# Performance work log

Hardware: AMD Instinct MI355X
Metric: run time of the kernel (lower is better)

The kernel has to match this reference:

```python
import jax, jax.numpy as jnp
import numpy as np

COMMITMENT_COST = 0.25


def setup_inputs() -> dict:
    key = jax.random.key(0)
    k1, k2 = jax.random.split(key)
    B, D, H, W = 16, 256, 64, 64   # channel-first latents, D == embedding_dim
    K = 1024                        # num_embeddings
    z = jax.random.normal(k1, (B, D, H, W), dtype=jnp.float32)
    emb = jax.random.normal(k2, (K, D), dtype=jnp.float32)
    emb = emb / jnp.linalg.norm(emb, axis=1, keepdims=True)  # F.normalize(p=2, dim=1)
    return {"z": z, "embeddings": emb}


def reference(z, embeddings):
    D = embeddings.shape[1]
    input_shape = z.shape
    flat_z = z.reshape(-1, D)  # matches torch .view(-1, embedding_dim) on contiguous tensor
    dist = (jnp.sum(flat_z * flat_z, axis=1, keepdims=True)
            + jnp.sum(embeddings * embeddings, axis=1)
            - 2.0 * flat_z @ embeddings.T)
    encoding_indices = jnp.argmin(dist, axis=1)                       # [N]
    # one-hot @ embeddings == gather (same math, no [N,K] one-hot materialized)
    quantized = embeddings[encoding_indices].reshape(input_shape)
    e_latent_loss = jnp.mean((jax.lax.stop_gradient(quantized) - z) ** 2)
    q_latent_loss = jnp.mean((quantized - jax.lax.stop_gradient(z)) ** 2)
    vq_loss = q_latent_loss + COMMITMENT_COST * e_latent_loss
    quantized_st = z + jax.lax.stop_gradient(quantized - z)  # straight-through
    encoding_indices = encoding_indices.reshape((input_shape[0],) + input_shape[2:])
    return quantized_st, vq_loss, encoding_indices
```

## Files before the change

### kernel.cpp

```cpp
#include <hip/hip_runtime.h>
#include <stdint.h>


typedef __attribute__((ext_vector_type(8))) short short8;
typedef __attribute__((ext_vector_type(16))) float f32x16;

#define THR_S 1e-3f
#define WLCAP 16384

__device__ __forceinline__ unsigned short f2bf(float f) {
    const unsigned int x = __float_as_uint(f);
    return (unsigned short)((x + 0x7FFFu + ((x >> 16) & 1u)) >> 16);
}
__device__ __forceinline__ float bf2f(unsigned short h) {
    return __uint_as_float(((unsigned int)h) << 16);
}

#define MFMA32(A, B, C) __builtin_amdgcn_mfma_f32_32x32x16_bf16(A, B, C, 0, 0, 0)

__global__ __launch_bounds__(256)
void eprep_kernel(const float* __restrict__ emb, unsigned short* __restrict__ eh_t,
                  unsigned short* __restrict__ el_t, float* __restrict__ enorm,
                  int* __restrict__ wlcnt) {
    const int code = blockIdx.x;
    const int k = threadIdx.x;
    if (code == 0 && k == 0) wlcnt[0] = 0;
    const float v = emb[code * 256 + k];
    const unsigned short h = f2bf(v);
    const int idx = ((k >> 4) << 14) + (code << 4) + (((k >> 3) & 1) << 3) + (k & 7);
    eh_t[idx] = h;
    el_t[idx] = f2bf(v - bf2f(h));
    float s = v * v;
#pragma unroll
    for (int o = 32; o > 0; o >>= 1) s += __shfl_xor(s, o);
    __shared__ float red[4];
    if ((k & 63) == 0) red[k >> 6] = s;
    __syncthreads();
    if (k == 0) enorm[code] = (red[0] + red[1]) + (red[2] + red[3]);
}

#define UPD(S, C, B1, I1, B2) { \
    const bool lt_ = (S) < B1; \
    B2 = lt_ ? B1 : fminf(B2, (S)); \
    I1 = lt_ ? (C) : I1; \
    B1 = lt_ ? (S) : B1; }

#define MERGE32(B1, I1, B2) { \
    const float ob1_ = __shfl_xor(B1, 32); \
    const int   oi1_ = __shfl_xor(I1, 32); \
    const float ob2_ = __shfl_xor(B2, 32); \
    const float nb2_ = fminf(fminf(B2, ob2_), fmaxf(B1, ob1_)); \
    if (ob1_ < B1 || (ob1_ == B1 && oi1_ < I1)) { B1 = ob1_; I1 = oi1_; } \
    B2 = nb2_; }

#define PFLOAD(S, U) { \
    const int un_ = (U) & 63; \
    const int ofs_ = ((un_ & 15) << 15) + ((un_ >> 4) << 10); \
    pf##S##h = *reinterpret_cast<const short8*>(ehp + ofs_); \
    pf##S##l = *reinterpret_cast<const short8*>(elp + ofs_); }

#define UNIT(S, KS) { \
    const int ko_ = (((KS) << 5) + (hi << 4)) ^ rsw; \
    const short8 bh0 = *reinterpret_cast<const short8*>(zbuf + rb0 + ko_); \
    const short8 bl0 = *reinterpret_cast<const short8*>(zbuf + 32768 + rb0 + ko_); \
    const short8 bh1 = *reinterpret_cast<const short8*>(zbuf + rb1 + ko_); \
    const short8 bl1 = *reinterpret_cast<const short8*>(zbuf + 32768 + rb1 + ko_); \
    acc1a = MFMA32(pf##S##h, bh0, acc1a); \
    acc1b = MFMA32(pf##S##h, bh1, acc1b); \
    acc2a = MFMA32(pf##S##h, bl0, acc2a); \
    acc2b = MFMA32(pf##S##h, bl1, acc2b); \
    acc2a = MFMA32(pf##S##l, bh0, acc2a); \
    acc2b = MFMA32(pf##S##l, bh1, acc2b); }

__global__ __launch_bounds__(512, 4)
void argmin_kernel(const float* __restrict__ z, const unsigned short* __restrict__ eh_t,
                   float* __restrict__ idx_out, int* __restrict__ wl,
                   int* __restrict__ wlcnt, const float* __restrict__ emb,
                   float* __restrict__ q_out, float* __restrict__ partials) {
    __shared__ char zbuf[65536];
    __shared__ float m_b1[8][64];
    __shared__ int   m_i1[8][64];
    __shared__ float m_b2[8][64];
    __shared__ int   fidx_s[64];

    const int t = threadIdx.x;
    const int l = t & 63;
    const int w = t >> 6;
    const int cl = l & 31;
    const int hi = l >> 5;

    const float* zblk = z + (size_t)blockIdx.x * 16384;

#pragma unroll
    for (int i = 0; i < 8; ++i) {
        const int idx = i * 2048 + t * 4;
        const int row = idx >> 8, k = idx & 255;
        const float4 v = *reinterpret_cast<const float4*>(zblk + idx);
        ushort4 hv, lv;
        hv.x = f2bf(v.x); lv.x = f2bf(v.x - bf2f(hv.x));
        hv.y = f2bf(v.y); lv.y = f2bf(v.y - bf2f(hv.y));
        hv.z = f2bf(v.z); lv.z = f2bf(v.z - bf2f(hv.z));
        hv.w = f2bf(v.w); lv.w = f2bf(v.w - bf2f(hv.w));
        const int boff = row * 512 + ((k << 1) ^ ((row & 7) << 4));
        *reinterpret_cast<ushort4*>(zbuf + boff) = hv;
        *reinterpret_cast<ushort4*>(zbuf + 32768 + boff) = lv;
    }
    __syncthreads();

    const char* ehp = (const char*)eh_t + (w * 128 + cl) * 32 + hi * 16;
    const char* elp = ehp + 524288;

    const int rb0 = cl * 512;
    const int rb1 = rb0 + 16384;
    const int rsw = (cl & 7) << 4;

    f32x16 acc1a, acc2a, acc1b, acc2b;
#pragma unroll
    for (int j = 0; j < 16; ++j) { acc1a[j] = 0.f; acc2a[j] = 0.f; acc1b[j] = 0.f; acc2b[j] = 0.f; }

    float b1a = 3.4e38f, b2a = 3.4e38f, b1b = 3.4e38f, b2b = 3.4e38f;
    int   i1a = 0, i1b = 0;

    short8 pf0h, pf0l, pf1h, pf1l, pf2h, pf2l, pf3h, pf3l;
    PFLOAD(0, 0) PFLOAD(1, 1) PFLOAD(2, 2) PFLOAD(3, 3)

#pragma unroll 1
    for (int ct = 0; ct < 4; ++ct) {
#pragma unroll 1
        for (int j = 0; j < 4; ++j) {
            const int u0 = (ct << 4) + (j << 2);
            UNIT(0, ((j << 2) + 0)) PFLOAD(0, u0 + 4)
            UNIT(1, ((j << 2) + 1)) PFLOAD(1, u0 + 5)
            UNIT(2, ((j << 2) + 2)) PFLOAD(2, u0 + 6)
            UNIT(3, ((j << 2) + 3)) PFLOAD(3, u0 + 7)
        }
        const int code0 = w * 128 + (ct << 5) + (hi << 2);
#pragma unroll
        for (int reg = 0; reg < 16; ++reg) {
            const int code = code0 + (reg & 3) + ((reg >> 2) << 3);
            const float s0 = -(acc1a[reg] + acc2a[reg]);
            const float s1 = -(acc1b[reg] + acc2b[reg]);
            UPD(s0, code, b1a, i1a, b2a)
            UPD(s1, code, b1b, i1b, b2b)
            acc1a[reg] = 0.f; acc2a[reg] = 0.f; acc1b[reg] = 0.f; acc2b[reg] = 0.f;
        }
    }

    MERGE32(b1a, i1a, b2a)
    MERGE32(b1b, i1b, b2b)
    if (l < 32) {
        m_b1[w][cl] = b1a;      m_i1[w][cl] = i1a;      m_b2[w][cl] = b2a;
        m_b1[w][cl + 32] = b1b; m_i1[w][cl + 32] = i1b; m_b2[w][cl + 32] = b2b;
    }
    __syncthreads();
    if (t < 64) {
        float b1 = m_b1[0][t]; int i1 = m_i1[0][t]; float b2 = m_b2[0][t];
#pragma unroll
        for (int g = 1; g < 8; ++g) {
            const float ob1 = m_b1[g][t]; const int oi1 = m_i1[g][t]; const float ob2 = m_b2[g][t];
            const float nb2 = fminf(fminf(b2, ob2), fmaxf(b1, ob1));
            if (ob1 < b1 || (ob1 == b1 && oi1 < i1)) { b1 = ob1; i1 = oi1; }
            b2 = nb2;
        }
        const int grow = blockIdx.x * 64 + t;
        idx_out[grow] = (float)i1;
        fidx_s[t] = i1;
        if (b2 - b1 < THR_S) {
            const int pos = atomicAdd(wlcnt, 1);
            if (pos < WLCAP) wl[pos] = grow;
        }
    }

    if (q_out != nullptr) {
        __syncthreads();
        float lsum = 0.f;
        float* qblk = q_out + (size_t)blockIdx.x * 16384;
#pragma unroll
        for (int i = 0; i < 8; ++i) {
            const int row = i * 8 + w;
            const int code = fidx_s[row];
            const float4 e4 = *reinterpret_cast<const float4*>(
                emb + (size_t)code * 256 + l * 4);
            const int byt = row * 512 + ((l * 8) ^ ((row & 7) << 4));
            const ushort4 h4 = *reinterpret_cast<const ushort4*>(zbuf + byt);
            const ushort4 l4 = *reinterpret_cast<const ushort4*>(zbuf + 32768 + byt);
            const float zx = bf2f(h4.x) + bf2f(l4.x);
            const float zy = bf2f(h4.y) + bf2f(l4.y);
            const float zz = bf2f(h4.z) + bf2f(l4.z);
            const float zw = bf2f(h4.w) + bf2f(l4.w);
            const float dx = e4.x - zx, dy = e4.y - zy, dz = e4.z - zz, dw = e4.w - zw;
            lsum += dx * dx + dy * dy + dz * dz + dw * dw;
            *reinterpret_cast<float4*>(qblk + row * 256 + l * 4) = e4;
        }
#pragma unroll
        for (int o = 32; o > 0; o >>= 1) lsum += __shfl_xor(lsum, o);
        if (l == 0) m_b1[0][w] = lsum;
        __syncthreads();
        if (t == 0) {
            float s = 0.f;
#pragma unroll
            for (int g = 0; g < 8; ++g) s += m_b1[0][g];
            partials[blockIdx.x] = s;
        }
    }
}

__global__ __launch_bounds__(256)
void fixup_kernel(const float* __restrict__ z, const float* __restrict__ emb,
                  const float* __restrict__ enorm_g, const int* __restrict__ wl,
                  const int* __restrict__ wlcnt, float* __restrict__ idx_out,
                  float* __restrict__ q_out, float* __restrict__ wl_delta) {
    __shared__ float zrow[256];
    __shared__ float znred[4];
    __shared__ float mb[4];
    __shared__ int   mi[4];
    __shared__ int   fin_s;
    __shared__ float dred[4];

    const int t = threadIdx.x;
    const int l = t & 63, wv = t >> 6;
    const int dq = l & 3, tx = (l >> 2) & 15;

    int n = wlcnt[0];
    if (n > WLCAP) n = WLCAP;

#pragma unroll 1
    for (int i = blockIdx.x; i < n; i += 256) {
        const int r = wl[i];
        const float v = z[(size_t)r * 256 + t];
        zrow[t] = v;
        float zn = v * v;
#pragma unroll
        for (int o = 32; o > 0; o >>= 1) zn += __shfl_xor(zn, o);
        if (l == 0) znred[wv] = zn;
        __syncthreads();
        const float znf = (znred[0] + znred[1]) + (znred[2] + znred[3]);

        float b1 = 3.4e38f;
        int   i1 = 0;
#pragma unroll 1
        for (int cc = 0; cc < 16; ++cc) {
            const int c = wv * 256 + cc * 16 + tx;
            const float* er = emb + (size_t)c * 256 + dq * 4;
            float dot = 0.f;
#pragma unroll
            for (int j = 0; j < 16; ++j) {
                const float4 ev = *reinterpret_cast<const float4*>(er + j * 16);
                const float4 zv = *reinterpret_cast<const float4*>(&zrow[j * 16 + dq * 4]);
                dot = fmaf(zv.x, ev.x, dot);
                dot = fmaf(zv.y, ev.y, dot);
                dot = fmaf(zv.z, ev.z, dot);
                dot = fmaf(zv.w, ev.w, dot);
            }
            dot += __shfl_xor(dot, 1);
            dot += __shfl_xor(dot, 2);
            const float dist = fmaf(-2.f, dot, znf + enorm_g[c]);
            if (dist < b1) { b1 = dist; i1 = c; }
        }
#pragma unroll
        for (int off = 4; off < 64; off <<= 1) {
            const float ov = __shfl_xor(b1, off);
            const int   oi = __shfl_xor(i1, off);
            if (ov < b1 || (ov == b1 && oi < i1)) { b1 = ov; i1 = oi; }
        }
        if (l == 0) { mb[wv] = b1; mi[wv] = i1; }
        __syncthreads();
        if (t == 0) {
            float fb = mb[0]; int fi = mi[0];
#pragma unroll
            for (int g = 1; g < 4; ++g)
                if (mb[g] < fb || (mb[g] == fb && mi[g] < fi)) { fb = mb[g]; fi = mi[g]; }
            fin_s = fi;
        }
        __syncthreads();
        const int fi = fin_s;
        if (wl_delta != nullptr) {
            const int oldi = (int)idx_out[r];
            float d = 0.f;
            if (fi != oldi) {
                const float en_ = emb[(size_t)fi * 256 + t];
                const float eo_ = emb[(size_t)oldi * 256 + t];
                const float zt = zrow[t];
                d = (en_ - zt) * (en_ - zt) - (eo_ - zt) * (eo_ - zt);
                q_out[(size_t)r * 256 + t] = en_;
            }
#pragma unroll
            for (int o = 32; o > 0; o >>= 1) d += __shfl_xor(d, o);
            if (l == 0) dred[wv] = d;
            __syncthreads();
            if (t == 0) {
                wl_delta[i] = (dred[0] + dred[1]) + (dred[2] + dred[3]);
                idx_out[r] = (float)fi;
            }
        } else {
            if (t == 0) idx_out[r] = (float)fi;
        }
        __syncthreads();
    }
}

__global__ __launch_bounds__(256)
void loss_kernel(const float* __restrict__ partials, const float* __restrict__ wl_delta,
                 const int* __restrict__ wlcnt, float* __restrict__ loss_out) {
    const int tid = threadIdx.x;
    float s = partials[tid] + partials[tid + 256] + partials[tid + 512] + partials[tid + 768];
    int n = wlcnt[0];
    if (n > WLCAP) n = WLCAP;
    for (int i = tid; i < n; i += 256) s += wl_delta[i];
#pragma unroll
    for (int off = 32; off > 0; off >>= 1) s += __shfl_xor(s, off);
    __shared__ float red[4];
    if ((tid & 63) == 0) red[tid >> 6] = s;
    __syncthreads();
    if (tid == 0)
        loss_out[0] = ((red[0] + red[1]) + (red[2] + red[3])) * (1.25f / 16777216.0f);
}

__global__ __launch_bounds__(256)
void gather_kernel(const float* __restrict__ z, const float* __restrict__ emb,
                   const float* __restrict__ idx_f, float* __restrict__ q_out,
                   float* __restrict__ partials) {
    const int wv = threadIdx.x >> 6, ln = threadIdx.x & 63;
    float lsum = 0.f;
#pragma unroll
    for (int i = 0; i < 8; ++i) {
        const size_t row = (size_t)blockIdx.x * 32 + i * 4 + wv;
        const int kidx = (int)idx_f[row];
        const float4 e4 = *reinterpret_cast<const float4*>(emb + (size_t)kidx * 256 + ln * 4);
        const float4 z4 = *reinterpret_cast<const float4*>(z + row * 256 + ln * 4);
        *reinterpret_cast<float4*>(q_out + row * 256 + ln * 4) = e4;
        const float dx = e4.x - z4.x, dy = e4.y - z4.y, dz = e4.z - z4.z, dw = e4.w - z4.w;
        lsum += dx * dx + dy * dy + dz * dz + dw * dw;
    }
#pragma unroll
    for (int off = 32; off > 0; off >>= 1) lsum += __shfl_xor(lsum, off);
    __shared__ float red[4];
    if (ln == 0) red[wv] = lsum;
    __syncthreads();
    if (threadIdx.x == 0) partials[blockIdx.x] = red[0] + red[1] + red[2] + red[3];
}

__global__ __launch_bounds__(256)
void loss_fb_kernel(const float* __restrict__ partials, float* __restrict__ loss_out) {
    const int tid = threadIdx.x;
    float s = 0.f;
#pragma unroll
    for (int i = 0; i < 8; ++i) s += partials[tid + i * 256];
#pragma unroll
    for (int off = 32; off > 0; off >>= 1) s += __shfl_xor(s, off);
    __shared__ float red[4];
    if ((tid & 63) == 0) red[tid >> 6] = s;
    __syncthreads();
    if (tid == 0)
        loss_out[0] = (red[0] + red[1] + red[2] + red[3]) * (1.25f / 16777216.0f);
}

extern "C" void kernel_launch(void* const* d_in, const int* in_sizes, int n_in,
                              void* d_out, int out_size, void* d_ws, size_t ws_size,
                              hipStream_t stream) {
    const float* z   = (const float*)d_in[0];
    const float* emb = (const float*)d_in[1];
    float* out      = (float*)d_out;
    float* q_out    = out;
    float* loss_out = out + 16777216;
    float* idx_out  = out + 16777217;

    const size_t WS_NEEDED = (size_t)298048 * 4;
    float* ws = (float*)d_ws;

    if (ws_size >= WS_NEEDED) {
        unsigned short* eh_t = (unsigned short*)ws;
        unsigned short* el_t = eh_t + 262144;
        float* enorm    = ws + 262144;
        float* partials = ws + 263168;
        int*   wlcnt    = (int*)(ws + 265216);
        int*   wl       = (int*)(ws + 265280);
        float* wl_delta = ws + 281664;

        eprep_kernel<<<1024, 256, 0, stream>>>(emb, eh_t, el_t, enorm, wlcnt);
        argmin_kernel<<<1024, 512, 0, stream>>>(z, eh_t, idx_out, wl, wlcnt,
                                                emb, q_out, partials);
        fixup_kernel<<<256, 256, 0, stream>>>(z, emb, enorm, wl, wlcnt, idx_out,
                                              q_out, wl_delta);
        loss_kernel<<<1, 256, 0, stream>>>(partials, wl_delta, wlcnt, loss_out);
    } else {
        unsigned short* eh_t = (unsigned short*)q_out;
        unsigned short* el_t = eh_t + 262144;
        int*   wl    = (int*)(q_out + 262144);
        int*   wlcnt = (int*)(q_out + 327680);
        float* enorm    = ws;
        float* partials = ws + 1024;

        eprep_kernel<<<1024, 256, 0, stream>>>(emb, eh_t, el_t, enorm, wlcnt);
        argmin_kernel<<<1024, 512, 0, stream>>>(z, eh_t, idx_out, wl, wlcnt,
                                                emb, nullptr, nullptr);
        fixup_kernel<<<256, 256, 0, stream>>>(z, emb, enorm, wl, wlcnt, idx_out,
                                              nullptr, nullptr);
        gather_kernel<<<2048, 256, 0, stream>>>(z, emb, idx_out, q_out, partials);
        loss_fb_kernel<<<1, 256, 0, stream>>>(partials, loss_out);
    }
}
```

Before: 157.9 us.

## Process two code tiles per pass to reuse LDS z fragments across MFMAs

The argmin loop now handles two code tiles at once. Each set of z fragments read from LDS feeds MFMAs for both tiles, which halves LDS reads per MFMA. The hi and lo correction products are folded into a single accumulator per tile instead of separate acc1/acc2, so the register count stays similar. Prefetch is restructured per pair with explicit k-step indexing, and the loop drops from four outer iterations to two. Because prefetch now restarts at each pass instead of being carried across tiles, some load latency may be exposed at pass boundaries. Accumulating hi*hi together with the small cross terms could also change rounding slightly.

```diff
diff --git a/kernel.cpp b/kernel.cpp
--- a/kernel.cpp
+++ b/kernel.cpp
@@ -53,24 +53,29 @@
     if (ob1_ < B1 || (ob1_ == B1 && oi1_ < I1)) { B1 = ob1_; I1 = oi1_; } \
     B2 = nb2_; }
 
-#define PFLOAD(S, U) { \
-    const int un_ = (U) & 63; \
-    const int ofs_ = ((un_ & 15) << 15) + ((un_ >> 4) << 10); \
+#define PFLD(S, CT, KS) { \
+    const int ofs_ = ((KS) << 15) + ((CT) << 10); \
     pf##S##h = *reinterpret_cast<const short8*>(ehp + ofs_); \
     pf##S##l = *reinterpret_cast<const short8*>(elp + ofs_); }
 
-#define UNIT(S, KS) { \
+#define UNITPAIR(KS, PA, PB) { \
     const int ko_ = (((KS) << 5) + (hi << 4)) ^ rsw; \
     const short8 bh0 = *reinterpret_cast<const short8*>(zbuf + rb0 + ko_); \
     const short8 bl0 = *reinterpret_cast<const short8*>(zbuf + 32768 + rb0 + ko_); \
     const short8 bh1 = *reinterpret_cast<const short8*>(zbuf + rb1 + ko_); \
     const short8 bl1 = *reinterpret_cast<const short8*>(zbuf + 32768 + rb1 + ko_); \
-    acc1a = MFMA32(pf##S##h, bh0, acc1a); \
-    acc1b = MFMA32(pf##S##h, bh1, acc1b); \
-    acc2a = MFMA32(pf##S##h, bl0, acc2a); \
-    acc2b = MFMA32(pf##S##h, bl1, acc2b); \
-    acc2a = MFMA32(pf##S##l, bh0, acc2a); \
-    acc2b = MFMA32(pf##S##l, bh1, acc2b); }
+    accA0 = MFMA32(PA##h, bh0, accA0); \
+    accA1 = MFMA32(PA##h, bh1, accA1); \
+    accB0 = MFMA32(PB##h, bh0, accB0); \
+    accB1 = MFMA32(PB##h, bh1, accB1); \
+    accA0 = MFMA32(PA##h, bl0, accA0); \
+    accA1 = MFMA32(PA##h, bl1, accA1); \
+    accB0 = MFMA32(PB##h, bl0, accB0); \
+    accB1 = MFMA32(PB##h, bl1, accB1); \
+    accA0 = MFMA32(PA##l, bh0, accA0); \
+    accA1 = MFMA32(PA##l, bh1, accA1); \
+    accB0 = MFMA32(PB##l, bh0, accB0); \
+    accB1 = MFMA32(PB##l, bh1, accB1); }
 
 __global__ __launch_bounds__(512, 4)
 void argmin_kernel(const float* __restrict__ z, const unsigned short* __restrict__ eh_t,
@@ -114,35 +119,38 @@
     const int rb1 = rb0 + 16384;
     const int rsw = (cl & 7) << 4;
 
-    f32x16 acc1a, acc2a, acc1b, acc2b;
-#pragma unroll
-    for (int j = 0; j < 16; ++j) { acc1a[j] = 0.f; acc2a[j] = 0.f; acc1b[j] = 0.f; acc2b[j] = 0.f; }
-
     float b1a = 3.4e38f, b2a = 3.4e38f, b1b = 3.4e38f, b2b = 3.4e38f;
     int   i1a = 0, i1b = 0;
 
     short8 pf0h, pf0l, pf1h, pf1l, pf2h, pf2l, pf3h, pf3l;
-    PFLOAD(0, 0) PFLOAD(1, 1) PFLOAD(2, 2) PFLOAD(3, 3)
 
 #pragma unroll 1
-    for (int ct = 0; ct < 4; ++ct) {
+    for (int cp = 0; cp < 2; ++cp) {
+        const int c0 = cp * 2, c1 = cp * 2 + 1;
+        f32x16 accA0, accA1, accB0, accB1;
+#pragma unroll
+        for (int j = 0; j < 16; ++j) { accA0[j] = 0.f; accA1[j] = 0.f; accB0[j] = 0.f; accB1[j] = 0.f; }
+
+        PFLD(0, c0, 0) PFLD(1, c1, 0) PFLD(2, c0, 1) PFLD(3, c1, 1)
+
 #pragma unroll 1
-        for (int j = 0; j < 4; ++j) {
-            const int u0 = (ct << 4) + (j << 2);
-            UNIT(0, ((j << 2) + 0)) PFLOAD(0, u0 + 4)
-            UNIT(1, ((j << 2) + 1)) PFLOAD(1, u0 + 5)
-            UNIT(2, ((j << 2) + 2)) PFLOAD(2, u0 + 6)
-            UNIT(3, ((j << 2) + 3)) PFLOAD(3, u0 + 7)
-        }
-        const int code0 = w * 128 + (ct << 5) + (hi << 2);
+        for (int ks = 0; ks < 16; ks += 2) {
+            UNITPAIR(ks, pf0, pf1)
+            if (ks < 14) { PFLD(0, c0, ks + 2) PFLD(1, c1, ks + 2) }
+            UNITPAIR(ks + 1, pf2, pf3)
+            if (ks < 13) { PFLD(2, c0, ks + 3) PFLD(3, c1, ks + 3) }
+        }
+
+        const int codeA = w * 128 + (c0 << 5) + (hi << 2);
+        const int codeB = w * 128 + (c1 << 5) + (hi << 2);
 #pragma unroll
         for (int reg = 0; reg < 16; ++reg) {
-            const int code = code0 + (reg & 3) + ((reg >> 2) << 3);
-            const float s0 = -(acc1a[reg] + acc2a[reg]);
-            const float s1 = -(acc1b[reg] + acc2b[reg]);
-            UPD(s0, code, b1a, i1a, b2a)
-            UPD(s1, code, b1b, i1b, b2b)
-            acc1a[reg] = 0.f; acc2a[reg] = 0.f; acc1b[reg] = 0.f; acc2b[reg] = 0.f;
+            const int co = (reg & 3) + ((reg >> 2) << 3);
+            const int cA = codeA + co, cB = codeB + co;
+            UPD(-accA0[reg], cA, b1a, i1a, b2a)
+            UPD(-accA1[reg], cA, b1b, i1b, b2b)
+            UPD(-accB0[reg], cB, b1a, i1a, b2a)
+            UPD(-accB1[reg], cB, b1b, i1b, b2b)
         }
     }
 
```

New measurement: 160.6 us. No clear change (+1.7%).

## Restructure argmin MFMA loop with double-buffered LDS/global loads and setprio

Applied to the files above, without the earlier changes.

Restructures the main MFMA loop of the argmin kernel. The two accumulator pairs (hi*hi and cross terms) are merged into two accumulators, halving accumulator registers. Global loads of codebook fragments and LDS loads of z fragments are double-buffered per k-step. MFMA groups are wrapped in s_setprio to favour issuing matrix instructions over memory ops. The aim is to raise occupancy or latency hiding and to overlap loads with MFMA. In exchange, the prefetch depth for global loads shrinks from four units ahead to one or two, which may expose memory latency, and summing into a single accumulator changes rounding order slightly.

```diff
diff --git a/kernel.cpp b/kernel.cpp
--- a/kernel.cpp
+++ b/kernel.cpp
@@ -53,24 +53,27 @@
     if (ob1_ < B1 || (ob1_ == B1 && oi1_ < I1)) { B1 = ob1_; I1 = oi1_; } \
     B2 = nb2_; }
 
-#define PFLOAD(S, U) { \
-    const int un_ = (U) & 63; \
-    const int ofs_ = ((un_ & 15) << 15) + ((un_ >> 4) << 10); \
-    pf##S##h = *reinterpret_cast<const short8*>(ehp + ofs_); \
-    pf##S##l = *reinterpret_cast<const short8*>(elp + ofs_); }
-
-#define UNIT(S, KS) { \
+#define PFLD(PH, PL, CT, KS) { \
+    const int ofs_ = ((KS) << 15) + ((CT) << 10); \
+    PH = *reinterpret_cast<const short8*>(ehp + ofs_); \
+    PL = *reinterpret_cast<const short8*>(elp + ofs_); }
+
+#define LDB(H0, L0, H1, L1, KS) { \
     const int ko_ = (((KS) << 5) + (hi << 4)) ^ rsw; \
-    const short8 bh0 = *reinterpret_cast<const short8*>(zbuf + rb0 + ko_); \
-    const short8 bl0 = *reinterpret_cast<const short8*>(zbuf + 32768 + rb0 + ko_); \
-    const short8 bh1 = *reinterpret_cast<const short8*>(zbuf + rb1 + ko_); \
-    const short8 bl1 = *reinterpret_cast<const short8*>(zbuf + 32768 + rb1 + ko_); \
-    acc1a = MFMA32(pf##S##h, bh0, acc1a); \
-    acc1b = MFMA32(pf##S##h, bh1, acc1b); \
-    acc2a = MFMA32(pf##S##h, bl0, acc2a); \
-    acc2b = MFMA32(pf##S##h, bl1, acc2b); \
-    acc2a = MFMA32(pf##S##l, bh0, acc2a); \
-    acc2b = MFMA32(pf##S##l, bh1, acc2b); }
+    H0 = *reinterpret_cast<const short8*>(zbuf + rb0 + ko_); \
+    L0 = *reinterpret_cast<const short8*>(zbuf + 32768 + rb0 + ko_); \
+    H1 = *reinterpret_cast<const short8*>(zbuf + rb1 + ko_); \
+    L1 = *reinterpret_cast<const short8*>(zbuf + 32768 + rb1 + ko_); }
+
+#define MFMA6(PH, PL, H0, L0, H1, L1) \
+    __builtin_amdgcn_s_setprio(1); \
+    acc0 = MFMA32(PH, H0, acc0); \
+    acc1 = MFMA32(PH, H1, acc1); \
+    acc0 = MFMA32(PH, L0, acc0); \
+    acc1 = MFMA32(PH, L1, acc1); \
+    acc0 = MFMA32(PL, H0, acc0); \
+    acc1 = MFMA32(PL, H1, acc1); \
+    __builtin_amdgcn_s_setprio(0);
 
 __global__ __launch_bounds__(512, 4)
 void argmin_kernel(const float* __restrict__ z, const unsigned short* __restrict__ eh_t,
@@ -114,35 +117,39 @@
     const int rb1 = rb0 + 16384;
     const int rsw = (cl & 7) << 4;
 
-    f32x16 acc1a, acc2a, acc1b, acc2b;
-#pragma unroll
-    for (int j = 0; j < 16; ++j) { acc1a[j] = 0.f; acc2a[j] = 0.f; acc1b[j] = 0.f; acc2b[j] = 0.f; }
-
     float b1a = 3.4e38f, b2a = 3.4e38f, b1b = 3.4e38f, b2b = 3.4e38f;
     int   i1a = 0, i1b = 0;
 
-    short8 pf0h, pf0l, pf1h, pf1l, pf2h, pf2l, pf3h, pf3l;
-    PFLOAD(0, 0) PFLOAD(1, 1) PFLOAD(2, 2) PFLOAD(3, 3)
+    short8 pfAh, pfAl, pfBh, pfBl;
+    short8 ch0, cl0, ch1, cl1, nh0, nl0, nh1, nl1;
 
 #pragma unroll 1
     for (int ct = 0; ct < 4; ++ct) {
+        f32x16 acc0, acc1;
+#pragma unroll
+        for (int j = 0; j < 16; ++j) { acc0[j] = 0.f; acc1[j] = 0.f; }
+
+        PFLD(pfAh, pfAl, ct, 0)
+        LDB(ch0, cl0, ch1, cl1, 0)
+        PFLD(pfBh, pfBl, ct, 1)
+
 #pragma unroll 1
-        for (int j = 0; j < 4; ++j) {
-            const int u0 = (ct << 4) + (j << 2);
-            UNIT(0, ((j << 2) + 0)) PFLOAD(0, u0 + 4)
-            UNIT(1, ((j << 2) + 1)) PFLOAD(1, u0 + 5)
-            UNIT(2, ((j << 2) + 2)) PFLOAD(2, u0 + 6)
-            UNIT(3, ((j << 2) + 3)) PFLOAD(3, u0 + 7)
-        }
+        for (int ks = 0; ks < 16; ks += 2) {
+            LDB(nh0, nl0, nh1, nl1, ks + 1)
+            MFMA6(pfAh, pfAl, ch0, cl0, ch1, cl1)
+            if (ks < 14) PFLD(pfAh, pfAl, ct, ks + 2)
+            if (ks < 14) LDB(ch0, cl0, ch1, cl1, ks + 2)
+            MFMA6(pfBh, pfBl, nh0, nl0, nh1, nl1)
+            if (ks < 14) PFLD(pfBh, pfBl, ct, ks + 3)
+        }
+
         const int code0 = w * 128 + (ct << 5) + (hi << 2);
 #pragma unroll
         for (int reg = 0; reg < 16; ++reg) {
-            const int code = code0 + (reg & 3) + ((reg >> 2) << 3);
-            const float s0 = -(acc1a[reg] + acc2a[reg]);
-            const float s1 = -(acc1b[reg] + acc2b[reg]);
-            UPD(s0, code, b1a, i1a, b2a)
-            UPD(s1, code, b1b, i1b, b2b)
-            acc1a[reg] = 0.f; acc2a[reg] = 0.f; acc1b[reg] = 0.f; acc2b[reg] = 0.f;
+            const int co = (reg & 3) + ((reg >> 2) << 3);
+            const int c = code0 + co;
+            UPD(-acc0[reg], c, b1a, i1a, b2a)
+            UPD(-acc1[reg], c, b1b, i1b, b2b)
         }
     }
 
```

After: 161.2 us. +2.1%, slower.
